# Optimization experiments

Measured on AMD Instinct MI355X. Metric: run time of the kernel, lower is better.

The kernel has to match this reference:

```python
import jax, jax.numpy as jnp
import numpy as np

L, D, H, W = 4, 256, 8, 20      # num_layers, hidden_dim, num_heads, walk_length
G, NPG = 512, 128               # graphs, nodes per graph (equal-size -> dense batch is a reshape)
N = G * NPG                     # 65536 nodes
E = 8 * N                       # 524288 edges (avg degree 8)
DH = D // H                     # head dim 32
FF = 2 * D                      # GPSConv MLP hidden (Linear(D, 2D))
AV, BV = 128, 8                 # padded atom / bond vocab sizes (OGB-style encoders)


def setup_inputs() -> dict:
    key = jax.random.key(0)
    ks = iter(jax.random.split(key, 40))
    nrm = lambda *s: jax.random.normal(next(ks), s, jnp.float32) * 0.02
    zeros = lambda *s: jnp.zeros(s, jnp.float32)
    ones = lambda *s: jnp.ones(s, jnp.float32)
    return dict(
        x=jax.random.randint(next(ks), (N, 9), 0, 2),
        edge_index=jax.random.randint(next(ks), (2, E), 0, N),
        edge_attr=jax.random.randint(next(ks), (E, 3), 0, 2),
        batch=jnp.repeat(jnp.arange(G), NPG),
        pe=jax.random.normal(next(ks), (N, W), jnp.float32),
        atom_emb=nrm(9, AV, D), bond_emb=nrm(3, BV, D),
        pe_w=nrm(W, D), pe_b=zeros(D),
        gine_w1=nrm(L, D, D), gine_b1=zeros(L, D),
        gine_g1=ones(L, D), gine_be1=zeros(L, D),
        gine_w2=nrm(L, D, D), gine_b2=zeros(L, D),
        attn_wqkv=nrm(L, D, 3 * D), attn_bqkv=zeros(L, 3 * D),
        attn_wo=nrm(L, D, D), attn_bo=zeros(L, D),
        n1_g=ones(L, D), n1_b=zeros(L, D),
        n2_g=ones(L, D), n2_b=zeros(L, D),
        n3_g=ones(L, D), n3_b=zeros(L, D),
        mlp_w1=nrm(L, D, FF), mlp_b1=zeros(L, FF),
        mlp_w2=nrm(L, FF, D), mlp_b2=zeros(L, D),
    )


def _bn(z, g, b):
    # BatchNorm1d over the node axis (training-mode batch statistics)
    mu = z.mean(0)
    var = z.var(0)
    return (z - mu) * jax.lax.rsqrt(var + 1e-5) * g + b


def _forward(x, edge_index, edge_attr, batch, pe, atom_emb, bond_emb, pe_w, pe_b,
             gine_w1, gine_b1, gine_g1, gine_be1, gine_w2, gine_b2,
             attn_wqkv, attn_bqkv, attn_wo, attn_bo,
             n1_g, n1_b, n2_g, n2_b, n3_g, n3_b,
             mlp_w1, mlp_b1, mlp_w2, mlp_b2):
    # AtomEncoder / BondEncoder: sum of per-column embeddings; PE fusion
    h = atom_emb[jnp.arange(9), x].sum(1) + pe @ pe_w + pe_b      # [N, D]
    ea = bond_emb[jnp.arange(3), edge_attr].sum(1)                # [E, D]
    src, dst = edge_index[0], edge_index[1]
    for l in range(L):
        # --- GINEConv: gather -> relu(x_j + e) -> scatter-add -> MLP ---
        m = jax.nn.relu(h[src] + ea)                              # [E, D]
        agg = jax.ops.segment_sum(m, dst, num_segments=N)         # [N, D]
        z = h + agg                                               # eps = 0
        z = jax.nn.relu(_bn(z @ gine_w1[l] + gine_b1[l], gine_g1[l], gine_be1[l]))
        z = jax.nn.relu(z @ gine_w2[l] + gine_b2[l])
        h_local = _bn(z + h, n1_g[l], n1_b[l])                    # residual + norm1 (dropout off)
        # --- global multi-head self-attention per graph (dense batch) ---
        xd = h.reshape(G, NPG, D)
        qkv = xd @ attn_wqkv[l] + attn_bqkv[l]                    # [G, NPG, 3D]
        q, k, v = jnp.split(qkv, 3, axis=-1)
        q = q.reshape(G, NPG, H, DH).transpose(0, 2, 1, 3)        # [G, H, NPG, DH]
        k = k.reshape(G, NPG, H, DH).transpose(0, 2, 1, 3)
        v = v.reshape(G, NPG, H, DH).transpose(0, 2, 1, 3)
        scores = jnp.einsum('ghnd,ghmd->ghnm', q, k) / jnp.sqrt(jnp.float32(DH))
        attn = jax.nn.softmax(scores, axis=-1)                    # all nodes valid (equal-size graphs)
        o = jnp.einsum('ghnm,ghmd->ghnd', attn, v)
        o = o.transpose(0, 2, 1, 3).reshape(G, NPG, D) @ attn_wo[l] + attn_bo[l]
        h_attn = _bn(o.reshape(N, D) + h, n2_g[l], n2_b[l])       # residual + norm2
        # --- combine + feed-forward MLP + norm3 ---
        out = h_local + h_attn
        out = jax.nn.relu(out @ mlp_w1[l] + mlp_b1[l]) @ mlp_w2[l] + mlp_b2[l]
        h = _bn(out, n3_g[l], n3_b[l])
    return jax.ops.segment_sum(h, batch, num_segments=G)          # global_add_pool [G, D]


def reference(x, edge_index, edge_attr, batch, pe, atom_emb, bond_emb, pe_w, pe_b,
              gine_w1, gine_b1, gine_g1, gine_be1, gine_w2, gine_b2,
              attn_wqkv, attn_bqkv, attn_wo, attn_bo,
              n1_g, n1_b, n2_g, n2_b, n3_g, n3_b,
              mlp_w1, mlp_b1, mlp_w2, mlp_b2):
    return _forward(x, edge_index, edge_attr, batch, pe, atom_emb, bond_emb, pe_w, pe_b,
                    gine_w1, gine_b1, gine_g1, gine_be1, gine_w2, gine_b2,
                    attn_wqkv, attn_bqkv, attn_wo, attn_bo,
                    n1_g, n1_b, n2_g, n2_b, n3_g, n3_b,
                    mlp_w1, mlp_b1, mlp_w2, mlp_b2)
```

## Files before the change

### kernel.cpp

```cpp
#include <hip/hip_runtime.h>
#include <stdint.h>


#define NN   65536
#define EE   524288
#define DD   256
#define LL   4
#define GG   512
#define NPGx 128
#define FFF  512

typedef __attribute__((ext_vector_type(8))) short short8;
typedef __attribute__((ext_vector_type(8))) __bf16 bf16x8;
typedef __attribute__((ext_vector_type(4))) float f32x4;

__device__ __forceinline__ float b2f(unsigned short u){
  union {unsigned int i; float f;} z; z.i = ((unsigned int)u) << 16; return z.f;
}
__device__ __forceinline__ unsigned short f2b(float f){
  union {float f; unsigned int i;} z; z.f = f;
  unsigned int r = z.i + 0x7fff + ((z.i >> 16) & 1u);
  return (unsigned short)(r >> 16);
}

__device__ __forceinline__ void gld16(void* lds, const void* g){
  __builtin_amdgcn_global_load_lds(
      (const __attribute__((address_space(1))) void*)g,
      (__attribute__((address_space(3))) void*)lds, 16, 0, 0);
}


__global__ __launch_bounds__(256) void combo_k(const float* __restrict__ be,
                                               unsigned short* __restrict__ tab){
  int c = blockIdx.x, d = threadIdx.x;
  int a0 = c & 7, a1 = (c >> 3) & 7, a2 = (c >> 6) & 7;
  tab[c*DD + d] = f2b(be[a0*DD + d] + be[(8 + a1)*DD + d] + be[(16 + a2)*DD + d]);
}

__global__ __launch_bounds__(256) void hist_k(const int* __restrict__ ei,
                                              int* __restrict__ cnt){
  for (int i = blockIdx.x*256 + threadIdx.x; i < EE; i += gridDim.x*256)
    atomicAdd(&cnt[ei[EE + i]], 1);
}

__global__ __launch_bounds__(1024) void scan_k(int* __restrict__ cnt,
                                               int* __restrict__ row_ptr){
  __shared__ int sd[1024];
  __shared__ int carry;
  int t = threadIdx.x;
  if (t == 0) carry = 0;
  __syncthreads();
  for (int base = 0; base < NN; base += 4096){
    int idx = base + t*4;
    int v0 = cnt[idx+0], v1 = cnt[idx+1], v2 = cnt[idx+2], v3 = cnt[idx+3];
    int s = v0 + v1 + v2 + v3;
    sd[t] = s; __syncthreads();
    for (int offd = 1; offd < 1024; offd <<= 1){
      int xv = (t >= offd) ? sd[t - offd] : 0;
      __syncthreads();
      sd[t] += xv;
      __syncthreads();
    }
    int excl = sd[t] - s + carry;
    row_ptr[idx+0] = excl;             cnt[idx+0] = excl;
    row_ptr[idx+1] = excl + v0;        cnt[idx+1] = excl + v0;
    row_ptr[idx+2] = excl + v0 + v1;   cnt[idx+2] = excl + v0 + v1;
    row_ptr[idx+3] = excl + v0+v1+v2;  cnt[idx+3] = excl + v0+v1+v2;
    __syncthreads();
    if (t == 0) carry += sd[1023];
    __syncthreads();
  }
  if (t == 0) row_ptr[NN] = carry;
}

__global__ __launch_bounds__(256) void fill_k(const int* __restrict__ ei,
                                              const int* __restrict__ ea,
                                              int* __restrict__ cursor,
                                              int* __restrict__ slot){
  for (int i = blockIdx.x*256 + threadIdx.x; i < EE; i += gridDim.x*256){
    int s  = ei[i];
    int dn = ei[EE + i];
    int a0 = ea[i*3+0], a1 = ea[i*3+1], a2 = ea[i*3+2];
    int cb = a0 | (a1 << 3) | (a2 << 6);
    int p = atomicAdd(&cursor[dn], 1);
    slot[p] = s | (cb << 16);
  }
}

__global__ __launch_bounds__(256) void twt_k(const float* __restrict__ w1,
                                             const float* __restrict__ w2,
                                             const float* __restrict__ wqkv,
                                             const float* __restrict__ wo,
                                             const float* __restrict__ m1,
                                             const float* __restrict__ m2,
                                             unsigned short* __restrict__ wt){
  __shared__ float tile[64][65];
  int l = blockIdx.x / 160;
  int r = blockIdx.x % 160;
  const float* src; unsigned short* dst; int K, Nsrc, t0;
  unsigned short* wl = wt + (size_t)l*655360;
  if (r < 16)      { src = w1  +(size_t)l*65536;  dst = wl;        K=256; Nsrc=256; t0=r; }
  else if (r < 32) { src = w2  +(size_t)l*65536;  dst = wl+65536;  K=256; Nsrc=256; t0=r-16; }
  else if (r < 80) { src = wqkv+(size_t)l*196608; dst = wl+131072; K=256; Nsrc=768; t0=r-32; }
  else if (r < 96) { src = wo  +(size_t)l*65536;  dst = wl+327680; K=256; Nsrc=256; t0=r-80; }
  else if (r < 128){ src = m1  +(size_t)l*131072; dst = wl+393216; K=256; Nsrc=512; t0=r-96; }
  else             { src = m2  +(size_t)l*131072; dst = wl+524288; K=512; Nsrc=256; t0=r-128; }
  int nkt = K >> 6;
  int tn = t0 / nkt, tk = t0 % nkt;
  int rr = threadIdx.x >> 6, cc = threadIdx.x & 63;
  for (int p = 0; p < 64; p += 4)
    tile[p+rr][cc] = src[(size_t)(tk*64 + p + rr)*Nsrc + tn*64 + cc];
  __syncthreads();
  for (int p = 0; p < 64; p += 4)
    dst[(size_t)(tn*64 + p + rr)*K + tk*64 + cc] = f2b(tile[cc][p+rr]);
}

__global__ __launch_bounds__(256) void enc_k(const int* __restrict__ x,
                                             const float* __restrict__ pe,
                                             const float* __restrict__ atom_emb,
                                             const float* __restrict__ pe_w,
                                             const float* __restrict__ pe_b,
                                             unsigned short* __restrict__ hb){
  int wv = blockIdx.x*4 + (threadIdx.x >> 6);
  int lane = threadIdx.x & 63;
  int d0 = lane*4;
  f32x4 pw[20];
  #pragma unroll
  for (int t = 0; t < 20; t++) pw[t] = *(const f32x4*)(pe_w + t*DD + d0);
  f32x4 pb = *(const f32x4*)(pe_b + d0);
  int n0 = wv*8;
  for (int n = n0; n < n0 + 8; n++){
    f32x4 acc = pb;
    #pragma unroll
    for (int i = 0; i < 9; i++){
      int xi = x[n*9 + i];
      acc += *(const f32x4*)(atom_emb + (size_t)(i*128 + xi)*DD + d0);
    }
    #pragma unroll
    for (int t = 0; t < 20; t++) acc += pe[n*20 + t] * pw[t];
    ushort4 o;
    o.x = f2b(acc[0]); o.y = f2b(acc[1]); o.z = f2b(acc[2]); o.w = f2b(acc[3]);
    *(ushort4*)(hb + (size_t)n*DD + d0) = o;
  }
}

__global__ __launch_bounds__(256) void gather_k(const unsigned short* __restrict__ hb,
                                                const int* __restrict__ row_ptr,
                                                const int* __restrict__ slot,
                                                const unsigned short* __restrict__ combo,
                                                unsigned short* __restrict__ t1){
  int w = threadIdx.x >> 6, lane = threadIdx.x & 63;
  int n = blockIdx.x*4 + w;
  int half = lane >> 5, l32 = lane & 31;
  int d0 = l32*8;
  int beg = row_ptr[n], end = row_ptr[n+1];
  float acc[8];
  #pragma unroll
  for (int u = 0; u < 8; u++) acc[u] = 0.f;
  for (int e = beg + half; e < end; e += 2){
    int s = slot[e];
    int src = s & 0xFFFF;
    int cb  = ((unsigned)s) >> 16;
    short8 hv = *(const short8*)(hb + (size_t)src*DD + d0);
    short8 cv = *(const short8*)(combo + (size_t)cb*DD + d0);
    #pragma unroll
    for (int u = 0; u < 8; u++)
      acc[u] += fmaxf(b2f((unsigned short)hv[u]) + b2f((unsigned short)cv[u]), 0.f);
  }
  #pragma unroll
  for (int u = 0; u < 8; u++) acc[u] += __shfl_xor(acc[u], 32, 64);
  if (half == 0){
    short8 hn = *(const short8*)(hb + (size_t)n*DD + d0);
    short8 o;
    #pragma unroll
    for (int u = 0; u < 8; u++) o[u] = (short)f2b(b2f((unsigned short)hn[u]) + acc[u]);
    *(short8*)(t1 + (size_t)n*DD + d0) = o;
  }
}

template<int PRO, bool RELU, bool RES, bool STATS>
__global__ __launch_bounds__(512, 4) void mgemm_k(
    const unsigned short* __restrict__ A,
    const unsigned short* __restrict__ A2,
    const unsigned short* __restrict__ Bt,
    const float* __restrict__ bias,
    const unsigned short* __restrict__ res,
    const float* __restrict__ stIn1, const float* __restrict__ gg1, const float* __restrict__ bb1,
    const float* __restrict__ stIn2, const float* __restrict__ gg2, const float* __restrict__ bb2,
    float* __restrict__ statsOut,
    unsigned short* __restrict__ C,
    int Nn, int K)
{
  __shared__ __align__(16) __bf16 SA[2][128*32];
  __shared__ __align__(16) __bf16 SB[2][256*32];
  __shared__ __align__(16) float scF1[256], shF1[256], scF2[256], shF2[256];

  const int tid  = threadIdx.x;
  const int wid  = tid >> 6, lane = tid & 63;
  const int row0 = blockIdx.x * 128, col0 = blockIdx.y * 256;
  const int wrr = wid >> 2, wcc = wid & 3;
  const int fr = lane & 15, fq = lane >> 4;
  const int srow = tid >> 2, sch = tid & 3;
  const int swc = sch ^ (srow & 3);
  const int nt = K >> 5;

  if (PRO >= 1 && tid < 256){
    float mu = stIn1[tid]*(1.f/NN);
    float var = stIn1[256+tid]*(1.f/NN) - mu*mu;
    float s = rsqrtf(var + 1e-5f) * gg1[tid];
    scF1[tid] = s; shF1[tid] = bb1[tid] - mu*s;
    if (PRO == 2){
      float mu2 = stIn2[tid]*(1.f/NN);
      float va2 = stIn2[256+tid]*(1.f/NN) - mu2*mu2;
      float s2 = rsqrtf(va2 + 1e-5f) * gg2[tid];
      scF2[tid] = s2; shF2[tid] = bb2[tid] - mu2*s2;
    }
  }

  f32x4 acc[4][4];
  #pragma unroll
  for (int i = 0; i < 4; i++)
    #pragma unroll
    for (int j = 0; j < 4; j++) acc[i][j] = f32x4{0.f,0.f,0.f,0.f};

  auto stageA = [&](int buf, int kt){
    gld16(&SA[buf][(wid*16)*32],
          A + (size_t)(row0 + srow)*K + kt + swc*8);
  };
  auto stageB = [&](int buf, int kt){
    #pragma unroll
    for (int rr = 0; rr < 2; rr++)
      gld16(&SB[buf][(wid*16 + rr*128)*32],
            Bt + (size_t)(col0 + srow + rr*128)*K + kt + swc*8);
  };

  short8 g1v, g4v;
  auto loadA = [&](int kt){
    g1v = *(const short8*)(A + (size_t)(row0 + srow)*K + kt + sch*8);
    if (PRO == 2) g4v = *(const short8*)(A2 + (size_t)(row0 + srow)*K + kt + sch*8);
  };
  auto dswA = [&](int buf, int kt){
    f32x4 s1a = *(const f32x4*)&scF1[kt + sch*8];
    f32x4 s1b = *(const f32x4*)&scF1[kt + sch*8 + 4];
    f32x4 h1a = *(const f32x4*)&shF1[kt + sch*8];
    f32x4 h1b = *(const f32x4*)&shF1[kt + sch*8 + 4];
    f32x4 s2a, s2b, h2a, h2b;
    if (PRO == 2){
      s2a = *(const f32x4*)&scF2[kt + sch*8];
      s2b = *(const f32x4*)&scF2[kt + sch*8 + 4];
      h2a = *(const f32x4*)&shF2[kt + sch*8];
      h2b = *(const f32x4*)&shF2[kt + sch*8 + 4];
    }
    short8 o;
    #pragma unroll
    for (int u = 0; u < 8; u++){
      float sc = (u < 4) ? s1a[u&3] : s1b[u&3];
      float sh = (u < 4) ? h1a[u&3] : h1b[u&3];
      float v = b2f((unsigned short)g1v[u]) * sc + sh;
      if (PRO == 1) v = fmaxf(v, 0.f);
      if (PRO == 2){
        float sc2 = (u < 4) ? s2a[u&3] : s2b[u&3];
        float sh2 = (u < 4) ? h2a[u&3] : h2b[u&3];
        v += b2f((unsigned short)g4v[u]) * sc2 + sh2;
      }
      o[u] = (short)f2b(v);
    }
    *(short8*)&SA[buf][srow*32 + swc*8] = o;
  };

  if (PRO == 0){
    stageA(0, 0); stageB(0, 0);
  } else {
    loadA(0); stageB(0, 0);
    __syncthreads();
  }

  int cur = 0;
  for (int t = 0; t < nt; t++){
    if (PRO == 0){
      __syncthreads();
      if (t+1 < nt){ stageA(cur^1, (t+1)*32); stageB(cur^1, (t+1)*32); }
    } else {
      dswA(cur, t*32);
      __syncthreads();
      if (t+1 < nt){ loadA((t+1)*32); stageB(cur^1, (t+1)*32); }
    }
    {
      int kc = (fq ^ (fr & 3)) * 8;
      bf16x8 a[4], b[4];
      #pragma unroll
      for (int i = 0; i < 4; i++)
        a[i] = *(const bf16x8*)&SA[cur][(wrr*64 + 16*i + fr)*32 + kc];
      #pragma unroll
      for (int j = 0; j < 4; j++)
        b[j] = *(const bf16x8*)&SB[cur][(wcc*64 + 16*j + fr)*32 + kc];
      #pragma unroll
      for (int i = 0; i < 4; i++)
        #pragma unroll
        for (int j = 0; j < 4; j++)
          acc[i][j] = __builtin_amdgcn_mfma_f32_16x16x32_bf16(a[i], b[j], acc[i][j], 0, 0, 0);
    }
    cur ^= 1;
  }

  float bj[4];
  #pragma unroll
  for (int j = 0; j < 4; j++) bj[j] = bias[col0 + wcc*64 + 16*j + fr];

  #pragma unroll
  for (int i = 0; i < 4; i++){
    #pragma unroll
    for (int j = 0; j < 4; j++){
      int col = col0 + wcc*64 + 16*j + fr;
      #pragma unroll
      for (int r = 0; r < 4; r++){
        int row = row0 + wrr*64 + 16*i + fq*4 + r;
        float y = acc[i][j][r] + bj[j];
        if constexpr (RELU) y = fmaxf(y, 0.f);
        if constexpr (RES)  y += b2f(res[(size_t)row*256 + col]);
        acc[i][j][r] = y;
        C[(size_t)row*Nn + col] = f2b(y);
      }
    }
  }

  if constexpr (STATS){
    float* csA = (float*)&SA[0][0];
    float* cqA = csA + 256;
    __syncthreads();
    if (tid < 256){ csA[tid] = 0.f; cqA[tid] = 0.f; }
    __syncthreads();
    #pragma unroll
    for (int j = 0; j < 4; j++){
      float ps = 0.f, pq = 0.f;
      #pragma unroll
      for (int i = 0; i < 4; i++)
        #pragma unroll
        for (int r = 0; r < 4; r++){ float v = acc[i][j][r]; ps += v; pq += v*v; }
      ps += __shfl_xor(ps, 16, 64); pq += __shfl_xor(pq, 16, 64);
      ps += __shfl_xor(ps, 32, 64); pq += __shfl_xor(pq, 32, 64);
      if (lane < 16){
        atomicAdd(&csA[wcc*64 + 16*j + fr], ps);
        atomicAdd(&cqA[wcc*64 + 16*j + fr], pq);
      }
    }
    __syncthreads();
    if (tid < 256){
      atomicAdd(&statsOut[col0 + tid],       csA[tid]);
      atomicAdd(&statsOut[256 + col0 + tid], cqA[tid]);
    }
  }
}

__global__ __launch_bounds__(256) void bnf_k(unsigned short* __restrict__ t,
                                             const float* __restrict__ st,
                                             const float* __restrict__ g,
                                             const float* __restrict__ b){
  __shared__ float sc[256], sh[256];
  int tid = threadIdx.x;
  {
    float mu  = st[tid] * (1.f/NN);
    float var = st[256+tid] * (1.f/NN) - mu*mu;
    float s   = rsqrtf(var + 1e-5f) * g[tid];
    sc[tid] = s; sh[tid] = b[tid] - mu*s;
  }
  __syncthreads();
  size_t base = ((size_t)blockIdx.x*256 + tid)*8;
  int c0 = (int)(base & 255);
  short8 v = *(const short8*)(t + base);
  short8 o;
  #pragma unroll
  for (int u = 0; u < 8; u++){
    float f = b2f((unsigned short)v[u])*sc[c0+u] + sh[c0+u];
    o[u] = (short)f2b(f);
  }
  *(short8*)(t + base) = o;
}

__global__ __launch_bounds__(64) void attn_k(const unsigned short* __restrict__ qkv,
                                             unsigned short* __restrict__ o_out){
  int g  = blockIdx.x >> 3;
  int hh = blockIdx.x & 7;
  int lane = threadIdx.x;
  int fr = lane & 15, fq = lane >> 4;
  __shared__ __align__(16) unsigned short Vt[32*136];
  __shared__ __align__(16) unsigned short P[16*128];

  const unsigned short* qb = qkv + (size_t)g*128*768 + hh*32;
  const unsigned short* kb = qb + 256;
  const unsigned short* vb = qb + 512;

  #pragma unroll
  for (int h2 = 0; h2 < 2; h2++){
    int n = lane + 64*h2;
    const short8* vr = (const short8*)(vb + (size_t)n*768);
    #pragma unroll
    for (int c = 0; c < 4; c++){
      short8 v = vr[c];
      #pragma unroll
      for (int u = 0; u < 8; u++)
        Vt[(c*8+u)*136 + n] = (unsigned short)v[u];
    }
  }
  bf16x8 bk[8];
  #pragma unroll
  for (int j = 0; j < 8; j++)
    bk[j] = *(const bf16x8*)(kb + (size_t)(16*j + fr)*768 + fq*8);
  __syncthreads();
  bf16x8 bv[4][2];
  #pragma unroll
  for (int kk = 0; kk < 4; kk++)
    #pragma unroll
    for (int j2 = 0; j2 < 2; j2++)
      bv[kk][j2] = *(const bf16x8*)&Vt[(16*j2 + fr)*136 + kk*32 + fq*8];

  const float SCALE = 0.17677669529663687f;
  for (int m0 = 0; m0 < 128; m0 += 16){
    bf16x8 aq = *(const bf16x8*)(qb + (size_t)(m0 + fr)*768 + fq*8);
    f32x4 s[8];
    #pragma unroll
    for (int j = 0; j < 8; j++)
      s[j] = __builtin_amdgcn_mfma_f32_16x16x32_bf16(aq, bk[j], f32x4{0.f,0.f,0.f,0.f}, 0, 0, 0);
    float linv[4];
    #pragma unroll
    for (int r = 0; r < 4; r++){
      float mx = s[0][r];
      #pragma unroll
      for (int j = 1; j < 8; j++) mx = fmaxf(mx, s[j][r]);
      mx = fmaxf(mx, __shfl_xor(mx, 1, 64));
      mx = fmaxf(mx, __shfl_xor(mx, 2, 64));
      mx = fmaxf(mx, __shfl_xor(mx, 4, 64));
      mx = fmaxf(mx, __shfl_xor(mx, 8, 64));
      float sum = 0.f;
      #pragma unroll
      for (int j = 0; j < 8; j++){
        float p = __expf((s[j][r] - mx) * SCALE);
        unsigned short pb = f2b(p);
        s[j][r] = b2f(pb);
        sum += s[j][r];
      }
      sum += __shfl_xor(sum, 1, 64);
      sum += __shfl_xor(sum, 2, 64);
      sum += __shfl_xor(sum, 4, 64);
      sum += __shfl_xor(sum, 8, 64);
      linv[r] = 1.f / sum;
    }
    #pragma unroll
    for (int j = 0; j < 8; j++)
      #pragma unroll
      for (int r = 0; r < 4; r++){
        int row = fq*4 + r;
        int col = (16*j + fr) ^ ((row & 7) << 3);
        P[row*128 + col] = f2b(s[j][r]);
      }
    __syncthreads();
    f32x4 o0 = {0.f,0.f,0.f,0.f}, o1 = {0.f,0.f,0.f,0.f};
    #pragma unroll
    for (int kk = 0; kk < 4; kk++){
      bf16x8 pa = *(const bf16x8*)&P[fr*128 + ((kk*32 + fq*8) ^ ((fr & 7) << 3))];
      o0 = __builtin_amdgcn_mfma_f32_16x16x32_bf16(pa, bv[kk][0], o0, 0, 0, 0);
      o1 = __builtin_amdgcn_mfma_f32_16x16x32_bf16(pa, bv[kk][1], o1, 0, 0, 0);
    }
    #pragma unroll
    for (int r = 0; r < 4; r++){
      int row = g*128 + m0 + fq*4 + r;
      unsigned short* dst = o_out + (size_t)row*DD + hh*32;
      dst[fr]      = f2b(o0[r]*linv[r]);
      dst[16 + fr] = f2b(o1[r]*linv[r]);
    }
    __syncthreads();
  }
}

__global__ __launch_bounds__(256) void pool_k(const unsigned short* __restrict__ hb,
                                              float* __restrict__ out){
  int g = blockIdx.x, d = threadIdx.x;
  float acc = 0.f;
  for (int r = 0; r < NPGx; r++) acc += b2f(hb[(size_t)(g*NPGx + r)*DD + d]);
  out[g*DD + d] = acc;
}


extern "C" void kernel_launch(void* const* d_in, const int* in_sizes, int n_in,
                              void* d_out, int out_size, void* d_ws, size_t ws_size,
                              hipStream_t stream)
{
  const int*   x         = (const int*)  d_in[0];
  const int*   ei        = (const int*)  d_in[1];
  const int*   ea        = (const int*)  d_in[2];
  const float* pe        = (const float*)d_in[4];
  const float* atom_emb  = (const float*)d_in[5];
  const float* bond_emb  = (const float*)d_in[6];
  const float* pe_w      = (const float*)d_in[7];
  const float* pe_b      = (const float*)d_in[8];
  const float* gine_w1   = (const float*)d_in[9];
  const float* gine_b1   = (const float*)d_in[10];
  const float* gine_g1   = (const float*)d_in[11];
  const float* gine_be1  = (const float*)d_in[12];
  const float* gine_w2   = (const float*)d_in[13];
  const float* gine_b2   = (const float*)d_in[14];
  const float* attn_wqkv = (const float*)d_in[15];
  const float* attn_bqkv = (const float*)d_in[16];
  const float* attn_wo   = (const float*)d_in[17];
  const float* attn_bo   = (const float*)d_in[18];
  const float* n1_g      = (const float*)d_in[19];
  const float* n1_b      = (const float*)d_in[20];
  const float* n2_g      = (const float*)d_in[21];
  const float* n2_b      = (const float*)d_in[22];
  const float* n3_g      = (const float*)d_in[23];
  const float* n3_b      = (const float*)d_in[24];
  const float* mlp_w1    = (const float*)d_in[25];
  const float* mlp_b1    = (const float*)d_in[26];
  const float* mlp_w2    = (const float*)d_in[27];
  const float* mlp_b2    = (const float*)d_in[28];
  float* out = (float*)d_out;

  char* wsp = (char*)d_ws;
  size_t off = 0;
  auto alloc = [&](size_t bytes)->void*{
    void* p = wsp + off; off += (bytes + 255) & ~(size_t)255; return p;
  };
  unsigned short* hb  = (unsigned short*)alloc((size_t)NN*DD*2);
  unsigned short* t1  = (unsigned short*)alloc((size_t)NN*DD*2);
  unsigned short* t2  = (unsigned short*)alloc((size_t)NN*DD*2);
  unsigned short* t4  = (unsigned short*)alloc((size_t)NN*DD*2);
  unsigned short* big = (unsigned short*)alloc((size_t)NN*768*2);
  unsigned short* wt  = (unsigned short*)alloc((size_t)LL*655360*2);
  unsigned short* combo = (unsigned short*)alloc((size_t)512*DD*2);
  int*   row_ptr = (int*)  alloc((size_t)(NN+1)*4);
  int*   cursor  = (int*)  alloc((size_t)NN*4);
  int*   slot    = (int*)  alloc((size_t)EE*4);
  float* stats   = (float*)alloc((size_t)LL*4*2*DD*4);
  if (off > ws_size) return;

  hipMemsetAsync(stats,  0, (size_t)LL*4*2*DD*4, stream);
  hipMemsetAsync(cursor, 0, (size_t)NN*4, stream);
  combo_k<<<512, 256, 0, stream>>>(bond_emb, combo);
  twt_k  <<<LL*160, 256, 0, stream>>>(gine_w1, gine_w2, attn_wqkv, attn_wo,
                                      mlp_w1, mlp_w2, wt);
  hist_k <<<512, 256, 0, stream>>>(ei, cursor);
  scan_k <<<1, 1024, 0, stream>>>(cursor, row_ptr);
  fill_k <<<512, 256, 0, stream>>>(ei, ea, cursor, slot);
  enc_k  <<<2048, 256, 0, stream>>>(x, pe, atom_emb, pe_w, pe_b, hb);

  for (int l = 0; l < LL; l++){
    unsigned short* wl = wt + (size_t)l*655360;
    const float* b1   = gine_b1   + l*DD;
    const float* b2   = gine_b2   + l*DD;
    const float* bqkv = attn_bqkv + l*768;
    const float* bo   = attn_bo   + l*DD;
    const float* mb1  = mlp_b1    + l*FFF;
    const float* mb2  = mlp_b2    + l*DD;
    float* S0 = stats + (l*4+0)*2*DD;
    float* S1 = stats + (l*4+1)*2*DD;
    float* S2 = stats + (l*4+2)*2*DD;
    float* S3 = stats + (l*4+3)*2*DD;

    gather_k<<<NN/4, 256, 0, stream>>>(hb, row_ptr, slot, combo, t1);
    mgemm_k<0,false,false,true><<<dim3(512,1), 512, 0, stream>>>(
        t1, nullptr, wl + 0, b1, nullptr,
        nullptr,nullptr,nullptr, nullptr,nullptr,nullptr, S0, t2, 256, 256);
    mgemm_k<1,true,true,true><<<dim3(512,1), 512, 0, stream>>>(
        t2, nullptr, wl + 65536, b2, hb,
        S0, gine_g1 + l*DD, gine_be1 + l*DD, nullptr,nullptr,nullptr, S1, t1, 256, 256);
    mgemm_k<0,false,false,false><<<dim3(512,3), 512, 0, stream>>>(
        hb, nullptr, wl + 131072, bqkv, nullptr,
        nullptr,nullptr,nullptr, nullptr,nullptr,nullptr, nullptr, big, 768, 256);
    attn_k<<<GG*8, 64, 0, stream>>>(big, t2);
    mgemm_k<0,false,true,true><<<dim3(512,1), 512, 0, stream>>>(
        t2, nullptr, wl + 327680, bo, hb,
        nullptr,nullptr,nullptr, nullptr,nullptr,nullptr, S2, t4, 256, 256);
    mgemm_k<2,true,false,false><<<dim3(512,2), 512, 0, stream>>>(
        t1, t4, wl + 393216, mb1, nullptr,
        S1, n1_g + l*DD, n1_b + l*DD, S2, n2_g + l*DD, n2_b + l*DD, nullptr, big, 512, 256);
    mgemm_k<0,false,false,true><<<dim3(512,1), 512, 0, stream>>>(
        big, nullptr, wl + 524288, mb2, nullptr,
        nullptr,nullptr,nullptr, nullptr,nullptr,nullptr, S3, hb, 256, 512);
    bnf_k<<<NN*DD/2048, 256, 0, stream>>>(hb, S3, n3_g + l*DD, n3_b + l*DD);
  }
  pool_k<<<GG, 256, 0, stream>>>(hb, out);
}
```

Measured before the change: 1.654 ms.

## Triple-buffer GEMM loads, unroll edge gather, pack four heads per attention block

The plain GEMM path now uses a three-stage LDS ring with explicit vmcnt waits and one barrier per k-step, to overlap global loads with MFMA. The gather loop processes two edges per iteration to expose more memory parallelism. The attention kernel runs four heads per 256-thread block with per-wave LDS buffers, removing block-wide barriers. The larger LDS footprint of the GEMM may reduce occupancy.

```diff
diff --git a/kernel.cpp b/kernel.cpp
--- a/kernel.cpp
+++ b/kernel.cpp
@@ -157,12 +157,24 @@
   float acc[8];
   #pragma unroll
   for (int u = 0; u < 8; u++) acc[u] = 0.f;
-  for (int e = beg + half; e < end; e += 2){
+  int e = beg + half;
+  for (; e + 2 < end; e += 4){
+    int sA = slot[e], sB = slot[e+2];
+    short8 hvA = *(const short8*)(hb + (size_t)(sA & 0xFFFF)*DD + d0);
+    short8 cvA = *(const short8*)(combo + (size_t)(((unsigned)sA) >> 16)*DD + d0);
+    short8 hvB = *(const short8*)(hb + (size_t)(sB & 0xFFFF)*DD + d0);
+    short8 cvB = *(const short8*)(combo + (size_t)(((unsigned)sB) >> 16)*DD + d0);
+    #pragma unroll
+    for (int u = 0; u < 8; u++)
+      acc[u] += fmaxf(b2f((unsigned short)hvA[u]) + b2f((unsigned short)cvA[u]), 0.f);
+    #pragma unroll
+    for (int u = 0; u < 8; u++)
+      acc[u] += fmaxf(b2f((unsigned short)hvB[u]) + b2f((unsigned short)cvB[u]), 0.f);
+  }
+  for (; e < end; e += 2){
     int s = slot[e];
-    int src = s & 0xFFFF;
-    int cb  = ((unsigned)s) >> 16;
-    short8 hv = *(const short8*)(hb + (size_t)src*DD + d0);
-    short8 cv = *(const short8*)(combo + (size_t)cb*DD + d0);
+    short8 hv = *(const short8*)(hb + (size_t)(s & 0xFFFF)*DD + d0);
+    short8 cv = *(const short8*)(combo + (size_t)(((unsigned)s) >> 16)*DD + d0);
     #pragma unroll
     for (int u = 0; u < 8; u++)
       acc[u] += fmaxf(b2f((unsigned short)hv[u]) + b2f((unsigned short)cv[u]), 0.f);
@@ -191,8 +203,8 @@
     unsigned short* __restrict__ C,
     int Nn, int K)
 {
-  __shared__ __align__(16) __bf16 SA[2][128*32];
-  __shared__ __align__(16) __bf16 SB[2][256*32];
+  __shared__ __align__(16) __bf16 SA[3][128*32];
+  __shared__ __align__(16) __bf16 SB[3][256*32];
   __shared__ __align__(16) float scF1[256], shF1[256], scF2[256], shF2[256];
 
   const int tid  = threadIdx.x;
@@ -234,73 +246,77 @@
             Bt + (size_t)(col0 + srow + rr*128)*K + kt + swc*8);
   };
 
-  short8 g1v, g4v;
-  auto loadA = [&](int kt){
-    g1v = *(const short8*)(A + (size_t)(row0 + srow)*K + kt + sch*8);
-    if (PRO == 2) g4v = *(const short8*)(A2 + (size_t)(row0 + srow)*K + kt + sch*8);
+  auto compute = [&](int buf){
+    int kc = (fq ^ (fr & 3)) * 8;
+    bf16x8 a[4], b[4];
+    #pragma unroll
+    for (int i = 0; i < 4; i++)
+      a[i] = *(const bf16x8*)&SA[buf][(wrr*64 + 16*i + fr)*32 + kc];
+    #pragma unroll
+    for (int j = 0; j < 4; j++)
+      b[j] = *(const bf16x8*)&SB[buf][(wcc*64 + 16*j + fr)*32 + kc];
+    #pragma unroll
+    for (int i = 0; i < 4; i++)
+      #pragma unroll
+      for (int j = 0; j < 4; j++)
+        acc[i][j] = __builtin_amdgcn_mfma_f32_16x16x32_bf16(a[i], b[j], acc[i][j], 0, 0, 0);
   };
-  auto dswA = [&](int buf, int kt){
-    f32x4 s1a = *(const f32x4*)&scF1[kt + sch*8];
-    f32x4 s1b = *(const f32x4*)&scF1[kt + sch*8 + 4];
-    f32x4 h1a = *(const f32x4*)&shF1[kt + sch*8];
-    f32x4 h1b = *(const f32x4*)&shF1[kt + sch*8 + 4];
-    f32x4 s2a, s2b, h2a, h2b;
-    if (PRO == 2){
-      s2a = *(const f32x4*)&scF2[kt + sch*8];
-      s2b = *(const f32x4*)&scF2[kt + sch*8 + 4];
-      h2a = *(const f32x4*)&shF2[kt + sch*8];
-      h2b = *(const f32x4*)&shF2[kt + sch*8 + 4];
-    }
-    short8 o;
-    #pragma unroll
-    for (int u = 0; u < 8; u++){
-      float sc = (u < 4) ? s1a[u&3] : s1b[u&3];
-      float sh = (u < 4) ? h1a[u&3] : h1b[u&3];
-      float v = b2f((unsigned short)g1v[u]) * sc + sh;
-      if (PRO == 1) v = fmaxf(v, 0.f);
+
+  if constexpr (PRO == 0){
+    stageA(0, 0);       stageB(0, 0);
+    stageA(1, 32);      stageB(1, 32);
+    for (int t = 0; t < nt; t++){
+      if (t + 1 < nt) asm volatile("s_waitcnt vmcnt(3)" ::: "memory");
+      else            asm volatile("s_waitcnt vmcnt(0)" ::: "memory");
+      __builtin_amdgcn_s_barrier();
+      __builtin_amdgcn_sched_barrier(0);
+      if (t + 2 < nt){ stageA((t+2)%3, (t+2)*32); stageB((t+2)%3, (t+2)*32); }
+      compute(t % 3);
+    }
+  } else {
+    short8 g1v, g4v;
+    auto loadA = [&](int kt){
+      g1v = *(const short8*)(A + (size_t)(row0 + srow)*K + kt + sch*8);
+      if (PRO == 2) g4v = *(const short8*)(A2 + (size_t)(row0 + srow)*K + kt + sch*8);
+    };
+    auto dswA = [&](int buf, int kt){
+      f32x4 s1a = *(const f32x4*)&scF1[kt + sch*8];
+      f32x4 s1b = *(const f32x4*)&scF1[kt + sch*8 + 4];
+      f32x4 h1a = *(const f32x4*)&shF1[kt + sch*8];
+      f32x4 h1b = *(const f32x4*)&shF1[kt + sch*8 + 4];
+      f32x4 s2a, s2b, h2a, h2b;
       if (PRO == 2){
-        float sc2 = (u < 4) ? s2a[u&3] : s2b[u&3];
-        float sh2 = (u < 4) ? h2a[u&3] : h2b[u&3];
-        v += b2f((unsigned short)g4v[u]) * sc2 + sh2;
+        s2a = *(const f32x4*)&scF2[kt + sch*8];
+        s2b = *(const f32x4*)&scF2[kt + sch*8 + 4];
+        h2a = *(const f32x4*)&shF2[kt + sch*8];
+        h2b = *(const f32x4*)&shF2[kt + sch*8 + 4];
       }
-      o[u] = (short)f2b(v);
-    }
-    *(short8*)&SA[buf][srow*32 + swc*8] = o;
-  };
-
-  if (PRO == 0){
-    stageA(0, 0); stageB(0, 0);
-  } else {
+      short8 o;
+      #pragma unroll
+      for (int u = 0; u < 8; u++){
+        float sc = (u < 4) ? s1a[u&3] : s1b[u&3];
+        float sh = (u < 4) ? h1a[u&3] : h1b[u&3];
+        float v = b2f((unsigned short)g1v[u]) * sc + sh;
+        if (PRO == 1) v = fmaxf(v, 0.f);
+        if (PRO == 2){
+          float sc2 = (u < 4) ? s2a[u&3] : s2b[u&3];
+          float sh2 = (u < 4) ? h2a[u&3] : h2b[u&3];
+          v += b2f((unsigned short)g4v[u]) * sc2 + sh2;
+        }
+        o[u] = (short)f2b(v);
+      }
+      *(short8*)&SA[buf][srow*32 + swc*8] = o;
+    };
     loadA(0); stageB(0, 0);
     __syncthreads();
-  }
-
-  int cur = 0;
-  for (int t = 0; t < nt; t++){
-    if (PRO == 0){
-      __syncthreads();
-      if (t+1 < nt){ stageA(cur^1, (t+1)*32); stageB(cur^1, (t+1)*32); }
-    } else {
+    int cur = 0;
+    for (int t = 0; t < nt; t++){
       dswA(cur, t*32);
       __syncthreads();
       if (t+1 < nt){ loadA((t+1)*32); stageB(cur^1, (t+1)*32); }
-    }
-    {
-      int kc = (fq ^ (fr & 3)) * 8;
-      bf16x8 a[4], b[4];
-      #pragma unroll
-      for (int i = 0; i < 4; i++)
-        a[i] = *(const bf16x8*)&SA[cur][(wrr*64 + 16*i + fr)*32 + kc];
-      #pragma unroll
-      for (int j = 0; j < 4; j++)
-        b[j] = *(const bf16x8*)&SB[cur][(wcc*64 + 16*j + fr)*32 + kc];
-      #pragma unroll
-      for (int i = 0; i < 4; i++)
-        #pragma unroll
-        for (int j = 0; j < 4; j++)
-          acc[i][j] = __builtin_amdgcn_mfma_f32_16x16x32_bf16(a[i], b[j], acc[i][j], 0, 0, 0);
-    }
-    cur ^= 1;
+      compute(cur);
+      cur ^= 1;
+    }
   }
 
   float bj[4];
@@ -377,14 +393,15 @@
   *(short8*)(t + base) = o;
 }
 
-__global__ __launch_bounds__(64) void attn_k(const unsigned short* __restrict__ qkv,
-                                             unsigned short* __restrict__ o_out){
-  int g  = blockIdx.x >> 3;
-  int hh = blockIdx.x & 7;
-  int lane = threadIdx.x;
+__global__ __launch_bounds__(256) void attn_k(const unsigned short* __restrict__ qkv,
+                                              unsigned short* __restrict__ o_out){
+  int g   = blockIdx.x >> 1;
+  int wid = threadIdx.x >> 6;
+  int hh  = (blockIdx.x & 1)*4 + wid;
+  int lane = threadIdx.x & 63;
   int fr = lane & 15, fq = lane >> 4;
-  __shared__ __align__(16) unsigned short Vt[32*136];
-  __shared__ __align__(16) unsigned short P[16*128];
+  __shared__ __align__(16) unsigned short Vt[4][32*136];
+  __shared__ __align__(16) unsigned short P[4][16*128];
 
   const unsigned short* qb = qkv + (size_t)g*128*768 + hh*32;
   const unsigned short* kb = qb + 256;
@@ -399,20 +416,19 @@
       short8 v = vr[c];
       #pragma unroll
       for (int u = 0; u < 8; u++)
-        Vt[(c*8+u)*136 + n] = (unsigned short)v[u];
+        Vt[wid][(c*8+u)*136 + n] = (unsigned short)v[u];
     }
   }
   bf16x8 bk[8];
   #pragma unroll
   for (int j = 0; j < 8; j++)
     bk[j] = *(const bf16x8*)(kb + (size_t)(16*j + fr)*768 + fq*8);
-  __syncthreads();
   bf16x8 bv[4][2];
   #pragma unroll
   for (int kk = 0; kk < 4; kk++)
     #pragma unroll
     for (int j2 = 0; j2 < 2; j2++)
-      bv[kk][j2] = *(const bf16x8*)&Vt[(16*j2 + fr)*136 + kk*32 + fq*8];
+      bv[kk][j2] = *(const bf16x8*)&Vt[wid][(16*j2 + fr)*136 + kk*32 + fq*8];
 
   const float SCALE = 0.17677669529663687f;
   for (int m0 = 0; m0 < 128; m0 += 16){
@@ -451,13 +467,12 @@
       for (int r = 0; r < 4; r++){
         int row = fq*4 + r;
         int col = (16*j + fr) ^ ((row & 7) << 3);
-        P[row*128 + col] = f2b(s[j][r]);
+        P[wid][row*128 + col] = f2b(s[j][r]);
       }
-    __syncthreads();
     f32x4 o0 = {0.f,0.f,0.f,0.f}, o1 = {0.f,0.f,0.f,0.f};
     #pragma unroll
     for (int kk = 0; kk < 4; kk++){
-      bf16x8 pa = *(const bf16x8*)&P[fr*128 + ((kk*32 + fq*8) ^ ((fr & 7) << 3))];
+      bf16x8 pa = *(const bf16x8*)&P[wid][fr*128 + ((kk*32 + fq*8) ^ ((fr & 7) << 3))];
       o0 = __builtin_amdgcn_mfma_f32_16x16x32_bf16(pa, bv[kk][0], o0, 0, 0, 0);
       o1 = __builtin_amdgcn_mfma_f32_16x16x32_bf16(pa, bv[kk][1], o1, 0, 0, 0);
     }
@@ -468,7 +483,6 @@
       dst[fr]      = f2b(o0[r]*linv[r]);
       dst[16 + fr] = f2b(o1[r]*linv[r]);
     }
-    __syncthreads();
   }
 }
 
@@ -566,7 +580,7 @@
     mgemm_k<0,false,false,false><<<dim3(512,3), 512, 0, stream>>>(
         hb, nullptr, wl + 131072, bqkv, nullptr,
         nullptr,nullptr,nullptr, nullptr,nullptr,nullptr, nullptr, big, 768, 256);
-    attn_k<<<GG*8, 64, 0, stream>>>(big, t2);
+    attn_k<<<GG*2, 256, 0, stream>>>(big, t2);
     mgemm_k<0,false,true,true><<<dim3(512,1), 512, 0, stream>>>(
         t2, nullptr, wl + 327680, bo, hb,
         nullptr,nullptr,nullptr, nullptr,nullptr,nullptr, S2, t4, 256, 256);
```

New measurement: 1.573 ms. -4.9%, faster.
